# Kernel optimization log

Measured on AMD Instinct MI355X. Metric: run time of the kernel, lower is better.

Reference implementation:

```python
import jax, jax.numpy as jnp
import numpy as np

N = 8192          # total nodes (bipartite: first half left, second half right)
E = 65536         # raw edges
D = 256           # emb_dim
H = 8             # heads
HD = D // H       # head_dim = 32
EAD = 2           # edge_attr_dim


def _init(k, shape, fan_in):
    return (jax.random.normal(k, shape, jnp.float32) / np.sqrt(fan_in)).astype(jnp.float32)


def setup_inputs() -> dict:
    key = jax.random.key(0)
    ks = jax.random.split(key, 16)
    x = jax.random.normal(ks[0], (N, D), jnp.float32)
    src = jax.random.randint(ks[1], (E,), 0, N // 2, jnp.int32)
    dst = jax.random.randint(ks[2], (E,), N // 2, N, jnp.int32)
    edge_index = jnp.stack([src, dst])                       # [2, E]
    edge_attr = jax.random.uniform(ks[3], (E, EAD), jnp.float32)
    query_mask = jax.random.randint(ks[4], (E,), 0, 2, jnp.int32).astype(bool)
    return {
        "x": x,
        "edge_index": edge_index,
        "edge_attr": edge_attr,
        "query_mask": query_mask,
        "start_right": N // 2,
        "W_kqv": _init(ks[5], (D, 3 * D), D), "b_kqv": jnp.zeros((3 * D,), jnp.float32),
        "W_edge": _init(ks[6], (EAD, D), EAD), "b_edge": jnp.zeros((D,), jnp.float32),
        "W_att1": _init(ks[7], (3 * HD, HD), 3 * HD), "b_att1": jnp.zeros((HD,), jnp.float32),
        "W_att2": _init(ks[8], (HD, 1), HD), "b_att2": jnp.zeros((1,), jnp.float32),
        "W_out": _init(ks[9], (D, D), D), "b_out": jnp.zeros((D,), jnp.float32),
        "bn_gamma": jnp.ones((D,), jnp.float32), "bn_beta": jnp.zeros((D,), jnp.float32),
    }


def _build_graph(edge_index, query_mask, n):
    """Replicates MetaGNN.forward edge preprocessing (static, int-only)."""
    ei = np.asarray(edge_index)
    qm = np.asarray(query_mask).astype(bool)
    sup = np.where(~qm)[0]                                   # support edges
    # cat([edge_index[:, support], edge_index.flip(0)], dim=1)
    src = np.concatenate([ei[0, sup], ei[1]])
    dst = np.concatenate([ei[1, sup], ei[0]])
    attr_idx = np.concatenate([sup, np.arange(ei.shape[1])])
    # remove_self_loops
    keep = src != dst
    src, dst, attr_idx = src[keep], dst[keep], attr_idx[keep]
    # add_self_loops with fill_value [0, 0]
    loops = np.arange(n)
    src = np.concatenate([src, loops])
    dst = np.concatenate([dst, loops])
    return jnp.asarray(src), jnp.asarray(dst), jnp.asarray(attr_idx)


def _layer(x, src, dst, ea, W_kqv, b_kqv, W_edge, b_edge, W_att1, b_att1,
           W_att2, b_att2, W_out, b_out, bn_gamma, bn_beta):
    n = x.shape[0]
    kqv = x @ W_kqv + b_kqv                                  # [N, 3D]
    q = kqv[dst, :D].reshape(-1, H, HD)                      # x_i (target)
    k = kqv[src, D:2 * D].reshape(-1, H, HD) / np.sqrt(HD)   # x_j (source)
    v = kqv[src, 2 * D:].reshape(-1, H, HD)
    ef = jax.nn.relu((ea @ W_edge + b_edge).reshape(-1, H, HD))
    feat = jnp.concatenate([k, q, ef], axis=-1)              # [E, H, 3*HD]
    hdn = jax.nn.relu(jnp.einsum('ehf,fd->ehd', feat, W_att1) + b_att1)
    logits = (jnp.einsum('ehd,do->eho', hdn, W_att2) + b_att2)[..., 0]  # [E, H]
    # scatter-softmax over destination node segments
    m = jax.ops.segment_max(logits, dst, num_segments=n)
    a = jnp.exp(logits - m[dst])
    s = jax.ops.segment_sum(a, dst, num_segments=n)
    alpha = a / (s[dst] + 1e-16)                             # [E, H]
    msg = (alpha[..., None] * v).reshape(-1, D) @ W_out + b_out
    out = jax.ops.segment_sum(msg, dst, num_segments=n) + x  # aggr='add' + residual
    # BatchNorm1d (training-mode batch statistics, eps=1e-5)
    mu = out.mean(axis=0)
    var = out.var(axis=0)
    return (out - mu) / jnp.sqrt(var + 1e-5) * bn_gamma + bn_beta


def reference(x, edge_index, edge_attr, query_mask, start_right,
              W_kqv, b_kqv, W_edge, b_edge, W_att1, b_att1, W_att2, b_att2,
              W_out, b_out, bn_gamma, bn_beta):
    n = x.shape[0]
    src, dst, attr_idx = _build_graph(edge_index, query_mask, n)
    ea = jnp.concatenate(
        [edge_attr[attr_idx], jnp.zeros((n, edge_attr.shape[1]), edge_attr.dtype)], axis=0)
    return _layer(x, src, dst, ea, W_kqv, b_kqv, W_edge, b_edge,
                  W_att1, b_att1, W_att2, b_att2, W_out, b_out, bn_gamma, bn_beta)
```

## Files before the change

### kernel.cpp

```cpp
#include <hip/hip_runtime.h>

#define N_NODES 8192
#define E_RAW   65536
#define NSLOT   (2*E_RAW + N_NODES)
#define DEGCAP  48
#define L_ITER  4

typedef __attribute__((ext_vector_type(8)))  short bf16x8;
typedef __attribute__((ext_vector_type(4)))  short bf16x4;
typedef __attribute__((ext_vector_type(4)))  float f32x4;
typedef __attribute__((ext_vector_type(16))) float f32x16;
typedef unsigned short u16;

__device__ __forceinline__ u16 f2b(float f) {
  unsigned u = __float_as_uint(f);
  u = (u + 0x7FFFu + ((u >> 16) & 1u)) >> 16;
  return (u16)u;
}
__device__ __forceinline__ float b2f(u16 b) {
  return __uint_as_float(((unsigned)b) << 16);
}

__global__ __launch_bounds__(256) void setup_k(
    const float* __restrict__ x, u16* __restrict__ xb,
    const float* __restrict__ W_kqv, const float* __restrict__ b_kqv,
    const float* __restrict__ W_att1, const float* __restrict__ b_att1,
    const float* __restrict__ W_edge, const float* __restrict__ b_edge,
    const float* __restrict__ W_out,
    u16* __restrict__ BcatT, float* __restrict__ biascat,
    u16* __restrict__ wa1t, u16* __restrict__ WoutT, float* __restrict__ beW,
    int4* __restrict__ zbase)
{
  __shared__ float tile[64][65];
  const float inv_sqrt_hd = 0.17677669529663687f;
  int bx = blockIdx.x, t = threadIdx.x;

  if (bx < 2048) {
    int i = bx * 256 + t;
    float4 v = ((const float4*)x)[i];
    ushort4 o;
    o.x = f2b(v.x); o.y = f2b(v.y); o.z = f2b(v.z); o.w = f2b(v.w);
    ((ushort4*)xb)[i] = o;
    return;
  }
  if (bx < 2836) {
    int c = bx - 2048;
    int i = t;
    if (c < 768) {
      float v;
      if (c < 256) {
        int h = c >> 5, d2 = c & 31;
        float s = 0.f;
        #pragma unroll
        for (int j = 0; j < 32; ++j)
          s += W_kqv[i*768 + 256 + h*32 + j] * W_att1[j*32 + d2];
        v = s * inv_sqrt_hd;
      } else if (c < 512) {
        int c2 = c - 256; int h = c2 >> 5, d2 = c2 & 31;
        float s = 0.f;
        #pragma unroll
        for (int j = 0; j < 32; ++j)
          s += W_kqv[i*768 + h*32 + j] * W_att1[(32+j)*32 + d2];
        v = s;
      } else {
        v = W_kqv[i*768 + c];
      }
      BcatT[(size_t)c * 256 + i] = f2b(v);
      if (i == 0) {
        float bv;
        if (c < 256) {
          int h = c >> 5, d2 = c & 31;
          float s = 0.f;
          for (int j = 0; j < 32; ++j)
            s += b_kqv[256 + h*32 + j] * W_att1[j*32 + d2];
          bv = s * inv_sqrt_hd;
        } else if (c < 512) {
          int c2 = c - 256; int h = c2 >> 5, d2 = c2 & 31;
          float s = 0.f;
          for (int j = 0; j < 32; ++j)
            s += b_kqv[h*32 + j] * W_att1[(32+j)*32 + d2];
          bv = s + b_att1[c2 & 31];
        } else {
          bv = b_kqv[c];
        }
        biascat[c] = bv;
      }
    } else if (c < 772) {
      int idx = (c - 768) * 256 + i;
      int d2 = idx >> 5, j = idx & 31;
      wa1t[idx] = f2b(W_att1[(64 + j) * 32 + d2]);
    } else {
      int b = c - 772;
      int r0 = (b >> 2) * 64, c0 = (b & 3) * 64;
      for (int idx = i; idx < 4096; idx += 256) {
        int r = idx >> 6, cc = idx & 63;
        tile[r][cc] = W_out[(size_t)(r0 + r) * 256 + c0 + cc];
      }
      __syncthreads();
      for (int idx = i; idx < 4096; idx += 256) {
        int cc = idx >> 6, r = idx & 63;
        WoutT[(size_t)(c0 + cc) * 256 + r0 + r] = f2b(tile[r][cc]);
      }
    }
    return;
  }
  if (bx == 2836) {
    int h = t >> 5, d2 = t & 31;
    float s = 0.f;
    #pragma unroll
    for (int f = 0; f < 32; ++f)
      s += fmaxf(b_edge[h*32 + f], 0.f) * W_att1[(64 + f)*32 + d2];
    beW[h*32 + d2] = s;
    return;
  }
  int i = (bx - 2837) * 256 + t;
  if (i < 2176) zbase[i] = make_int4(0, 0, 0, 0);
}

__global__ __launch_bounds__(256) void gemm_scatter_k(
    const u16* __restrict__ xb, const u16* __restrict__ BcatT,
    const float* __restrict__ biascat, u16* __restrict__ nodeF,
    const int* __restrict__ ei, const int* __restrict__ qm,
    int* __restrict__ cnt, int* __restrict__ csr)
{
  int bx = blockIdx.x, t = threadIdx.x;
  if (bx < 768) {
    int lane = t & 63, wid = t >> 6;
    int cb = bx % 12, rb = bx / 12;
    int r0 = rb * 128 + wid * 32;
    int c0 = cb * 64;
    int lr = lane & 15, lk = (lane >> 4) * 8;
    f32x4 acc0[4] = {}, acc1[4] = {};
    for (int k0 = 0; k0 < 256; k0 += 32) {
      bf16x8 a0 = *(const bf16x8*)&xb[(size_t)(r0 + lr) * 256 + k0 + lk];
      bf16x8 a1 = *(const bf16x8*)&xb[(size_t)(r0 + 16 + lr) * 256 + k0 + lk];
      bf16x8 b0 = *(const bf16x8*)&BcatT[(size_t)(c0 + lr) * 256 + k0 + lk];
      bf16x8 b1 = *(const bf16x8*)&BcatT[(size_t)(c0 + 16 + lr) * 256 + k0 + lk];
      bf16x8 b2 = *(const bf16x8*)&BcatT[(size_t)(c0 + 32 + lr) * 256 + k0 + lk];
      bf16x8 b3 = *(const bf16x8*)&BcatT[(size_t)(c0 + 48 + lr) * 256 + k0 + lk];
      acc0[0] = __builtin_amdgcn_mfma_f32_16x16x32_bf16(a0, b0, acc0[0], 0, 0, 0);
      acc0[1] = __builtin_amdgcn_mfma_f32_16x16x32_bf16(a0, b1, acc0[1], 0, 0, 0);
      acc0[2] = __builtin_amdgcn_mfma_f32_16x16x32_bf16(a0, b2, acc0[2], 0, 0, 0);
      acc0[3] = __builtin_amdgcn_mfma_f32_16x16x32_bf16(a0, b3, acc0[3], 0, 0, 0);
      acc1[0] = __builtin_amdgcn_mfma_f32_16x16x32_bf16(a1, b0, acc1[0], 0, 0, 0);
      acc1[1] = __builtin_amdgcn_mfma_f32_16x16x32_bf16(a1, b1, acc1[1], 0, 0, 0);
      acc1[2] = __builtin_amdgcn_mfma_f32_16x16x32_bf16(a1, b2, acc1[2], 0, 0, 0);
      acc1[3] = __builtin_amdgcn_mfma_f32_16x16x32_bf16(a1, b3, acc1[3], 0, 0, 0);
    }
    int rbase = r0 + (lane >> 4) * 4;
    #pragma unroll
    for (int cc = 0; cc < 4; ++cc) {
      float bias = biascat[c0 + cc*16 + lr];
      #pragma unroll
      for (int r = 0; r < 4; ++r) {
        nodeF[(size_t)(rbase + r) * 768 + c0 + cc*16 + lr]      = f2b(acc0[cc][r] + bias);
        nodeF[(size_t)(rbase + 16 + r) * 768 + c0 + cc*16 + lr] = f2b(acc1[cc][r] + bias);
      }
    }
    return;
  }
  int slot = (bx - 768) * 256 + t;
  if (slot >= NSLOT) return;
  int src, dst;
  if (slot < E_RAW) {
    if (qm[slot] != 0) return;
    src = ei[slot]; dst = ei[E_RAW + slot];
  } else if (slot < 2*E_RAW) {
    int e = slot - E_RAW;
    src = ei[E_RAW + e]; dst = ei[e];
  } else {
    int n = slot - 2*E_RAW;
    src = n; dst = n;
  }
  int pos = atomicAdd(&cnt[dst], 1);
  if (pos < DEGCAP) csr[dst*DEGCAP + pos] = (slot << 13) | src;
}

__global__ __launch_bounds__(256) void logits_k(
    const int* __restrict__ ei, const int* __restrict__ qm,
    const float* __restrict__ eattr, const u16* __restrict__ nf,
    const u16* __restrict__ wa1t,
    const float* __restrict__ W_edge, const float* __restrict__ b_edge,
    const float* __restrict__ W_att2, const float* __restrict__ beW,
    float* __restrict__ lgd)
{
  __shared__ __align__(16) u16 kqls[4][16][8][40];

  int bx = blockIdx.x, t = threadIdx.x, lane = t & 63, wid = t >> 6;
  int col = lane & 31;
  int e = col >> 3, h = col & 7, hi = lane >> 5;

  float w2r[16];
  #pragma unroll
  for (int r = 0; r < 16; ++r)
    w2r[r] = W_att2[(r & 3) + 8*(r >> 2) + 4*hi];

  if (bx < 1024) {
    float ce0[16], ce1[16], cbe[16];
    #pragma unroll
    for (int i = 0; i < 8; ++i) {
      int fA = hi*8 + i, fB = 16 + hi*8 + i;
      ce0[i]   = W_edge[h*32 + fA];       ce0[8+i] = W_edge[h*32 + fB];
      ce1[i]   = W_edge[256 + h*32 + fA]; ce1[8+i] = W_edge[256 + h*32 + fB];
      cbe[i]   = b_edge[h*32 + fA];       cbe[8+i] = b_edge[h*32 + fB];
    }
    bf16x8 af0 = *(const bf16x8*)&wa1t[(lane & 31)*32 + hi*8];
    bf16x8 af1 = *(const bf16x8*)&wa1t[(lane & 31)*32 + 16 + hi*8];

    for (int it = 0; it < L_ITER; ++it) {
      int er0 = ((bx * L_ITER + it) * 4 + wid) * 4;
      int er = er0 + e;
      int eqm = qm[er];
      float2 ea = *(const float2*)&eattr[2*er];

      #pragma unroll
      for (int m = 0; m < 8; ++m) {
        int flat = m*64 + lane;
        int ri = flat >> 5, chunk = flat & 31;
        int ee = ri & 3, ty = ri >> 2;
        int erow = er0 + ee;
        int node = (ty & 1) ? ei[E_RAW + erow] : ei[erow];
        int koff = (ty >> 1) ? 256 : 0;
        bf16x8 v = *(const bf16x8*)&nf[(size_t)node*768 + koff + chunk*8];
        *(bf16x8*)&kqls[wid][ri][chunk >> 2][(chunk & 3)*8] = v;
      }

      bf16x8 bf0, bf1;
      #pragma unroll
      for (int i = 0; i < 8; ++i) {
        float v0 = fmaf(ea.x, ce0[i],   fmaf(ea.y, ce1[i],   cbe[i]));
        float v1 = fmaf(ea.x, ce0[8+i], fmaf(ea.y, ce1[8+i], cbe[8+i]));
        bf0[i] = (short)f2b(fmaxf(v0, 0.f));
        bf1[i] = (short)f2b(fmaxf(v1, 0.f));
      }
      f32x16 acc = {};
      acc = __builtin_amdgcn_mfma_f32_32x32x16_bf16(af0, bf0, acc, 0, 0, 0);
      acc = __builtin_amdgcn_mfma_f32_32x32x16_bf16(af1, bf1, acc, 0, 0, 0);

      __builtin_amdgcn_wave_barrier();

      float lg0 = 0.f, lg1 = 0.f;
      #pragma unroll
      for (int q = 0; q < 4; ++q) {
        int off = q*8 + 4*hi;
        bf16x4 k0 = *(const bf16x4*)&kqls[wid][e][h][off];
        bf16x4 q0 = *(const bf16x4*)&kqls[wid][12 + e][h][off];
        bf16x4 k1 = *(const bf16x4*)&kqls[wid][4 + e][h][off];
        bf16x4 q1 = *(const bf16x4*)&kqls[wid][8 + e][h][off];
        #pragma unroll
        for (int j = 0; j < 4; ++j) {
          int r = q*4 + j;
          float efw = acc[r];
          float p0 = efw + b2f((u16)k0[j]) + b2f((u16)q0[j]);
          float p1 = efw + b2f((u16)k1[j]) + b2f((u16)q1[j]);
          lg0 = fmaf(fmaxf(p0, 0.f), w2r[r], lg0);
          lg1 = fmaf(fmaxf(p1, 0.f), w2r[r], lg1);
        }
      }
      lg0 += __shfl_xor(lg0, 32);
      lg1 += __shfl_xor(lg1, 32);
      if (hi == 0) {
        if (eqm == 0) lgd[(size_t)er*8 + h] = lg0;
        lgd[(size_t)(E_RAW + er)*8 + h] = lg1;
      }
      __builtin_amdgcn_wave_barrier();
    }
  } else {
    float bew[16];
    #pragma unroll
    for (int r = 0; r < 16; ++r)
      bew[r] = beW[h*32 + (r & 3) + 8*(r >> 2) + 4*hi];

    for (int it = 0; it < L_ITER; ++it) {
      int n0 = (((bx - 1024) * L_ITER + it) * 4 + wid) * 4;
      int nn = n0 + e;
      #pragma unroll
      for (int m = 0; m < 4; ++m) {
        int flat = m*64 + lane;
        int ri = flat >> 5, chunk = flat & 31;
        int ee = ri & 3, ty = ri >> 2;
        int node = n0 + ee;
        bf16x8 v = *(const bf16x8*)&nf[(size_t)node*768 + (ty ? 256 : 0) + chunk*8];
        *(bf16x8*)&kqls[wid][ri][chunk >> 2][(chunk & 3)*8] = v;
      }
      __builtin_amdgcn_wave_barrier();
      float lg0 = 0.f;
      #pragma unroll
      for (int q = 0; q < 4; ++q) {
        int off = q*8 + 4*hi;
        bf16x4 k0 = *(const bf16x4*)&kqls[wid][e][h][off];
        bf16x4 q0 = *(const bf16x4*)&kqls[wid][4 + e][h][off];
        #pragma unroll
        for (int j = 0; j < 4; ++j) {
          int r = q*4 + j;
          float p = bew[r] + b2f((u16)k0[j]) + b2f((u16)q0[j]);
          lg0 = fmaf(fmaxf(p, 0.f), w2r[r], lg0);
        }
      }
      lg0 += __shfl_xor(lg0, 32);
      if (hi == 0) lgd[(size_t)(2*E_RAW + nn)*8 + h] = lg0;
      __builtin_amdgcn_wave_barrier();
    }
  }
}

__global__ __launch_bounds__(256) void aggr_k(const int* __restrict__ cnt,
                                              const int* __restrict__ csr,
                                              const float* __restrict__ lgd,
                                              const u16* __restrict__ nf,
                                              u16* __restrict__ aggb) {
  int t = threadIdx.x, lane = t & 63, wid = t >> 6;
  int n = blockIdx.x * 4 + wid;
  int deg = cnt[n]; if (deg > DEGCAP) deg = DEGCAP;

  float m = -3.4e38f, s = 0.f;
  for (int i = lane >> 3; i < deg; i += 8) {
    int pk = csr[n*DEGCAP + i];
    float val = lgd[(size_t)((unsigned)pk >> 13)*8 + (lane & 7)];
    float mn = fmaxf(m, val);
    s = s * __expf(m - mn) + __expf(val - mn);
    m = mn;
  }
  #pragma unroll
  for (int msk = 8; msk <= 32; msk <<= 1) {
    float mo = __shfl_xor(m, msk), so = __shfl_xor(s, msk);
    float mn = fmaxf(m, mo);
    s = s * __expf(m - mn) + so * __expf(mo - mn);
    m = mn;
  }
  float sinv = 1.f / (s + 1e-16f);
  int head = lane >> 3;
  float mh = __shfl(m, head);
  float sh = __shfl(sinv, head);

  float ac0 = 0.f, ac1 = 0.f, ac2 = 0.f, ac3 = 0.f;
  const u16* vb = nf + 512 + lane * 4;
  #pragma unroll 2
  for (int i = 0; i < deg; ++i) {
    int pk = csr[n*DEGCAP + i];
    int slot = (unsigned)pk >> 13, srcv = pk & 8191;
    float a = __expf(lgd[(size_t)slot*8 + head] - mh) * sh;
    bf16x4 v = *(const bf16x4*)&vb[(size_t)srcv * 768];
    ac0 = fmaf(a, b2f((u16)v[0]), ac0);
    ac1 = fmaf(a, b2f((u16)v[1]), ac1);
    ac2 = fmaf(a, b2f((u16)v[2]), ac2);
    ac3 = fmaf(a, b2f((u16)v[3]), ac3);
  }
  ushort4 o; o.x = f2b(ac0); o.y = f2b(ac1); o.z = f2b(ac2); o.w = f2b(ac3);
  *(ushort4*)&aggb[(size_t)n * 256 + lane * 4] = o;
}

__global__ __launch_bounds__(256) void gemmout_k(const u16* __restrict__ aggb,
                                                 const u16* __restrict__ WoutT,
                                                 const float* __restrict__ x,
                                                 const int* __restrict__ cnt,
                                                 const float* __restrict__ b_out,
                                                 float* __restrict__ out,
                                                 float* __restrict__ bnsum,
                                                 float* __restrict__ bnsq) {
  int t = threadIdx.x, lane = t & 63, wid = t >> 6;
  int r0 = (blockIdx.y * 4 + wid) * 32;
  int c0 = blockIdx.x * 32;
  int lr = lane & 15, lk = (lane >> 4) * 8;
  f32x4 acc00 = {0.f,0.f,0.f,0.f}, acc01 = {0.f,0.f,0.f,0.f};
  f32x4 acc10 = {0.f,0.f,0.f,0.f}, acc11 = {0.f,0.f,0.f,0.f};
  for (int k0 = 0; k0 < 256; k0 += 32) {
    bf16x8 a0 = *(const bf16x8*)&aggb[(size_t)(r0 + lr) * 256 + k0 + lk];
    bf16x8 a1 = *(const bf16x8*)&aggb[(size_t)(r0 + 16 + lr) * 256 + k0 + lk];
    bf16x8 b0 = *(const bf16x8*)&WoutT[(size_t)(c0 + lr) * 256 + k0 + lk];
    bf16x8 b1 = *(const bf16x8*)&WoutT[(size_t)(c0 + 16 + lr) * 256 + k0 + lk];
    acc00 = __builtin_amdgcn_mfma_f32_16x16x32_bf16(a0, b0, acc00, 0, 0, 0);
    acc01 = __builtin_amdgcn_mfma_f32_16x16x32_bf16(a0, b1, acc01, 0, 0, 0);
    acc10 = __builtin_amdgcn_mfma_f32_16x16x32_bf16(a1, b0, acc10, 0, 0, 0);
    acc11 = __builtin_amdgcn_mfma_f32_16x16x32_bf16(a1, b1, acc11, 0, 0, 0);
  }
  int colA = c0 + lr, colB = c0 + 16 + lr;
  float bA = b_out[colA], bB = b_out[colB];
  int rbase = r0 + (lane >> 4) * 4;
  float sA = 0.f, qA = 0.f, sB = 0.f, qB = 0.f;
  #pragma unroll
  for (int r = 0; r < 4; ++r) {
    int rowA = rbase + r, rowB = rbase + 16 + r;
    float degA = (float)cnt[rowA], degB = (float)cnt[rowB];
    float v00 = acc00[r] + x[(size_t)rowA * 256 + colA] + degA * bA;
    float v01 = acc01[r] + x[(size_t)rowA * 256 + colB] + degA * bB;
    float v10 = acc10[r] + x[(size_t)rowB * 256 + colA] + degB * bA;
    float v11 = acc11[r] + x[(size_t)rowB * 256 + colB] + degB * bB;
    out[(size_t)rowA * 256 + colA] = v00;
    out[(size_t)rowA * 256 + colB] = v01;
    out[(size_t)rowB * 256 + colA] = v10;
    out[(size_t)rowB * 256 + colB] = v11;
    sA += v00 + v10; qA += v00*v00 + v10*v10;
    sB += v01 + v11; qB += v01*v01 + v11*v11;
  }
  #pragma unroll
  for (int msk = 16; msk <= 32; msk <<= 1) {
    sA += __shfl_xor(sA, msk); qA += __shfl_xor(qA, msk);
    sB += __shfl_xor(sB, msk); qB += __shfl_xor(qB, msk);
  }
  if (lane < 16) {
    atomicAdd(&bnsum[colA], sA); atomicAdd(&bnsq[colA], qA);
    atomicAdd(&bnsum[colB], sB); atomicAdd(&bnsq[colB], qB);
  }
}

__global__ __launch_bounds__(256) void bnapply_k(float* __restrict__ out,
                                                 const float* __restrict__ bnsum,
                                                 const float* __restrict__ bnsq,
                                                 const float* __restrict__ gamma,
                                                 const float* __restrict__ beta) {
  int t = threadIdx.x;
  int c4 = t & 63;
  int r = blockIdx.x * 4 + (t >> 6);
  float4 s4 = ((const float4*)bnsum)[c4];
  float4 q4 = ((const float4*)bnsq)[c4];
  float4 g4 = ((const float4*)gamma)[c4];
  float4 b4 = ((const float4*)beta)[c4];
  float4 v = ((const float4*)out)[(size_t)r * 64 + c4];
  #pragma unroll
  for (int j = 0; j < 4; ++j) {
    float mu = (&s4.x)[j] * (1.f / 8192.f);
    float var = (&q4.x)[j] * (1.f / 8192.f) - mu*mu;
    float inv = rsqrtf(var + 1e-5f);
    (&v.x)[j] = ((&v.x)[j] - mu) * inv * (&g4.x)[j] + (&b4.x)[j];
  }
  ((float4*)out)[(size_t)r * 64 + c4] = v;
}

extern "C" void kernel_launch(void* const* d_in, const int* in_sizes, int n_in,
                              void* d_out, int out_size, void* d_ws, size_t ws_size,
                              hipStream_t stream) {
  (void)in_sizes; (void)n_in; (void)out_size; (void)ws_size;
  const float* x      = (const float*)d_in[0];
  const int*   ei     = (const int*)d_in[1];
  const float* eattr  = (const float*)d_in[2];
  const int*   qm     = (const int*)d_in[3];
  const float* W_kqv  = (const float*)d_in[5];
  const float* b_kqv  = (const float*)d_in[6];
  const float* W_edge = (const float*)d_in[7];
  const float* b_edge = (const float*)d_in[8];
  const float* W_att1 = (const float*)d_in[9];
  const float* b_att1 = (const float*)d_in[10];
  const float* W_att2 = (const float*)d_in[11];
  const float* W_out  = (const float*)d_in[13];
  const float* b_out  = (const float*)d_in[14];
  const float* gamma  = (const float*)d_in[15];
  const float* beta   = (const float*)d_in[16];
  float* out = (float*)d_out;

  char* w = (char*)d_ws;
  u16*    xb      = (u16*)w;     w += (size_t)N_NODES*256*2;
  u16*    BcatT   = (u16*)w;     w += (size_t)768*256*2;
  u16*    wa1t    = (u16*)w;     w += 1024*2;
  u16*    WoutT   = (u16*)w;     w += (size_t)256*256*2;
  u16*    nodeFb  = (u16*)w;     w += (size_t)N_NODES*768*2;
  float*  biascat = (float*)w;   w += 768*4;
  float*  beW     = (float*)w;   w += 256*4;
  u16*    aggb    = (u16*)w;     w += (size_t)N_NODES*256*2;
  int*    cnt     = (int*)w;     w += N_NODES*4;
  float*  bnsum   = (float*)w;   w += 256*4;
  float*  bnsq    = (float*)w;   w += 256*4;
  int*    csr     = (int*)w;     w += (size_t)N_NODES*DEGCAP*4;
  float*  lgd     = (float*)w;   w += (size_t)NSLOT*8*4;

  setup_k<<<2846, 256, 0, stream>>>(
      x, xb, W_kqv, b_kqv, W_att1, b_att1, W_edge, b_edge, W_out,
      BcatT, biascat, wa1t, WoutT, beW, (int4*)cnt);

  gemm_scatter_k<<<768 + (NSLOT + 255)/256, 256, 0, stream>>>(
      xb, BcatT, biascat, nodeFb, ei, qm, cnt, csr);

  logits_k<<<1024 + 128, 256, 0, stream>>>(ei, qm, eattr, nodeFb, wa1t,
                                           W_edge, b_edge, W_att2, beW, lgd);

  aggr_k<<<N_NODES/4, 256, 0, stream>>>(cnt, csr, lgd, nodeFb, aggb);

  gemmout_k<<<dim3(256/32, N_NODES/128), 256, 0, stream>>>(
      aggb, WoutT, x, cnt, b_out, out, bnsum, bnsq);

  bnapply_k<<<N_NODES/4, 256, 0, stream>>>(out, bnsum, bnsq, gamma, beta);
}
```

Measured before the change: 102.0 us.

## Prefetch gathers in logits and aggregation kernels, widen output GEMM tile

The logits kernel loads edge attributes and query flags up front and fetches the next iteration's node indices early, so gather latency overlaps compute. The aggregation kernel reads each node's CSR list once into registers, broadcasts entries by shuffle, and software-pipelines the next logit/value load. The output GEMM now computes 64 columns per wave, reusing A fragments across four B tiles and halving the grid. This costs more registers, which may reduce occupancy, and leaves fewer blocks for the GEMM.

```diff
diff --git a/kernel.cpp b/kernel.cpp
--- a/kernel.cpp
+++ b/kernel.cpp
@@ -207,24 +207,44 @@
     bf16x8 af0 = *(const bf16x8*)&wa1t[(lane & 31)*32 + hi*8];
     bf16x8 af1 = *(const bf16x8*)&wa1t[(lane & 31)*32 + 16 + hi*8];
 
+    int eqm_r[L_ITER]; float2 ea_r[L_ITER];
+    #pragma unroll
     for (int it = 0; it < L_ITER; ++it) {
-      int er0 = ((bx * L_ITER + it) * 4 + wid) * 4;
-      int er = er0 + e;
-      int eqm = qm[er];
-      float2 ea = *(const float2*)&eattr[2*er];
-
+      int er = ((bx * L_ITER + it) * 4 + wid) * 4 + e;
+      eqm_r[it] = qm[er];
+      ea_r[it] = *(const float2*)&eattr[2*er];
+    }
+
+    int nidx[2][8];
+    #pragma unroll
+    for (int m = 0; m < 8; ++m) {
+      int flat = m*64 + lane, ri = flat >> 5;
+      int ee = ri & 3, ty = ri >> 2;
+      int erow = ((bx * L_ITER + 0) * 4 + wid) * 4 + ee;
+      nidx[0][m] = (ty & 1) ? ei[E_RAW + erow] : ei[erow];
+    }
+
+    #pragma unroll
+    for (int it = 0; it < L_ITER; ++it) {
+      if (it + 1 < L_ITER) {
+        #pragma unroll
+        for (int m = 0; m < 8; ++m) {
+          int flat = m*64 + lane, ri = flat >> 5;
+          int ee = ri & 3, ty = ri >> 2;
+          int erow = ((bx * L_ITER + it + 1) * 4 + wid) * 4 + ee;
+          nidx[(it+1) & 1][m] = (ty & 1) ? ei[E_RAW + erow] : ei[erow];
+        }
+      }
       #pragma unroll
       for (int m = 0; m < 8; ++m) {
-        int flat = m*64 + lane;
-        int ri = flat >> 5, chunk = flat & 31;
-        int ee = ri & 3, ty = ri >> 2;
-        int erow = er0 + ee;
-        int node = (ty & 1) ? ei[E_RAW + erow] : ei[erow];
+        int flat = m*64 + lane, ri = flat >> 5, chunk = flat & 31;
+        int ty = ri >> 2;
         int koff = (ty >> 1) ? 256 : 0;
-        bf16x8 v = *(const bf16x8*)&nf[(size_t)node*768 + koff + chunk*8];
+        bf16x8 v = *(const bf16x8*)&nf[(size_t)nidx[it & 1][m]*768 + koff + chunk*8];
         *(bf16x8*)&kqls[wid][ri][chunk >> 2][(chunk & 3)*8] = v;
       }
 
+      float2 ea = ea_r[it];
       bf16x8 bf0, bf1;
       #pragma unroll
       for (int i = 0; i < 8; ++i) {
@@ -260,7 +280,8 @@
       lg0 += __shfl_xor(lg0, 32);
       lg1 += __shfl_xor(lg1, 32);
       if (hi == 0) {
-        if (eqm == 0) lgd[(size_t)er*8 + h] = lg0;
+        int er = ((bx * L_ITER + it) * 4 + wid) * 4 + e;
+        if (eqm_r[it] == 0) lgd[(size_t)er*8 + h] = lg0;
         lgd[(size_t)(E_RAW + er)*8 + h] = lg1;
       }
       __builtin_amdgcn_wave_barrier();
@@ -312,13 +333,22 @@
   int t = threadIdx.x, lane = t & 63, wid = t >> 6;
   int n = blockIdx.x * 4 + wid;
   int deg = cnt[n]; if (deg > DEGCAP) deg = DEGCAP;
-
+  int head = lane >> 3;
+
+  int pk = (lane < deg) ? csr[n*DEGCAP + lane] : 0;
+
+  int i0 = lane >> 3, hh = lane & 7;
+  int nit = (deg + 7) >> 3;
   float m = -3.4e38f, s = 0.f;
-  for (int i = lane >> 3; i < deg; i += 8) {
-    int pk = csr[n*DEGCAP + i];
-    float val = lgd[(size_t)((unsigned)pk >> 13)*8 + (lane & 7)];
+  for (int ii = 0; ii < nit; ++ii) {
+    int i = ii * 8 + i0;
+    int ic = (i < deg) ? i : 0;
+    int pki = __shfl(pk, ic);
+    float val = (i < deg)
+        ? lgd[(size_t)((unsigned)pki >> 13)*8 + hh] : -3.4e38f;
     float mn = fmaxf(m, val);
-    s = s * __expf(m - mn) + __expf(val - mn);
+    float addv = (i < deg) ? __expf(val - mn) : 0.f;
+    s = s * __expf(m - mn) + addv;
     m = mn;
   }
   #pragma unroll
@@ -329,18 +359,23 @@
     m = mn;
   }
   float sinv = 1.f / (s + 1e-16f);
-  int head = lane >> 3;
   float mh = __shfl(m, head);
   float sh = __shfl(sinv, head);
 
   float ac0 = 0.f, ac1 = 0.f, ac2 = 0.f, ac3 = 0.f;
   const u16* vb = nf + 512 + lane * 4;
-  #pragma unroll 2
+  int pk0 = __shfl(pk, 0);
+  float lg_pf = lgd[(size_t)((unsigned)pk0 >> 13)*8 + head];
+  bf16x4 v_pf = *(const bf16x4*)&vb[(size_t)(pk0 & 8191) * 768];
   for (int i = 0; i < deg; ++i) {
-    int pk = csr[n*DEGCAP + i];
-    int slot = (unsigned)pk >> 13, srcv = pk & 8191;
-    float a = __expf(lgd[(size_t)slot*8 + head] - mh) * sh;
-    bf16x4 v = *(const bf16x4*)&vb[(size_t)srcv * 768];
+    float lgv = lg_pf;
+    bf16x4 v = v_pf;
+    if (i + 1 < deg) {
+      int pkn = __shfl(pk, i + 1);
+      lg_pf = lgd[(size_t)((unsigned)pkn >> 13)*8 + head];
+      v_pf = *(const bf16x4*)&vb[(size_t)(pkn & 8191) * 768];
+    }
+    float a = __expf(lgv - mh) * sh;
     ac0 = fmaf(a, b2f((u16)v[0]), ac0);
     ac1 = fmaf(a, b2f((u16)v[1]), ac1);
     ac2 = fmaf(a, b2f((u16)v[2]), ac2);
@@ -359,48 +394,56 @@
                                                  float* __restrict__ bnsum,
                                                  float* __restrict__ bnsq) {
   int t = threadIdx.x, lane = t & 63, wid = t >> 6;
-  int r0 = (blockIdx.y * 4 + wid) * 32;
-  int c0 = blockIdx.x * 32;
+  int bx = blockIdx.x;
+  int cb = bx & 3, rb = bx >> 2;
+  int r0 = rb * 128 + wid * 32;
+  int c0 = cb * 64;
   int lr = lane & 15, lk = (lane >> 4) * 8;
-  f32x4 acc00 = {0.f,0.f,0.f,0.f}, acc01 = {0.f,0.f,0.f,0.f};
-  f32x4 acc10 = {0.f,0.f,0.f,0.f}, acc11 = {0.f,0.f,0.f,0.f};
+  f32x4 acc0[4] = {}, acc1[4] = {};
   for (int k0 = 0; k0 < 256; k0 += 32) {
     bf16x8 a0 = *(const bf16x8*)&aggb[(size_t)(r0 + lr) * 256 + k0 + lk];
     bf16x8 a1 = *(const bf16x8*)&aggb[(size_t)(r0 + 16 + lr) * 256 + k0 + lk];
     bf16x8 b0 = *(const bf16x8*)&WoutT[(size_t)(c0 + lr) * 256 + k0 + lk];
     bf16x8 b1 = *(const bf16x8*)&WoutT[(size_t)(c0 + 16 + lr) * 256 + k0 + lk];
-    acc00 = __builtin_amdgcn_mfma_f32_16x16x32_bf16(a0, b0, acc00, 0, 0, 0);
-    acc01 = __builtin_amdgcn_mfma_f32_16x16x32_bf16(a0, b1, acc01, 0, 0, 0);
-    acc10 = __builtin_amdgcn_mfma_f32_16x16x32_bf16(a1, b0, acc10, 0, 0, 0);
-    acc11 = __builtin_amdgcn_mfma_f32_16x16x32_bf16(a1, b1, acc11, 0, 0, 0);
-  }
-  int colA = c0 + lr, colB = c0 + 16 + lr;
-  float bA = b_out[colA], bB = b_out[colB];
+    bf16x8 b2 = *(const bf16x8*)&WoutT[(size_t)(c0 + 32 + lr) * 256 + k0 + lk];
+    bf16x8 b3 = *(const bf16x8*)&WoutT[(size_t)(c0 + 48 + lr) * 256 + k0 + lk];
+    acc0[0] = __builtin_amdgcn_mfma_f32_16x16x32_bf16(a0, b0, acc0[0], 0, 0, 0);
+    acc0[1] = __builtin_amdgcn_mfma_f32_16x16x32_bf16(a0, b1, acc0[1], 0, 0, 0);
+    acc0[2] = __builtin_amdgcn_mfma_f32_16x16x32_bf16(a0, b2, acc0[2], 0, 0, 0);
+    acc0[3] = __builtin_amdgcn_mfma_f32_16x16x32_bf16(a0, b3, acc0[3], 0, 0, 0);
+    acc1[0] = __builtin_amdgcn_mfma_f32_16x16x32_bf16(a1, b0, acc1[0], 0, 0, 0);
+    acc1[1] = __builtin_amdgcn_mfma_f32_16x16x32_bf16(a1, b1, acc1[1], 0, 0, 0);
+    acc1[2] = __builtin_amdgcn_mfma_f32_16x16x32_bf16(a1, b2, acc1[2], 0, 0, 0);
+    acc1[3] = __builtin_amdgcn_mfma_f32_16x16x32_bf16(a1, b3, acc1[3], 0, 0, 0);
+  }
   int rbase = r0 + (lane >> 4) * 4;
-  float sA = 0.f, qA = 0.f, sB = 0.f, qB = 0.f;
+  float degA[4], degB[4];
   #pragma unroll
   for (int r = 0; r < 4; ++r) {
-    int rowA = rbase + r, rowB = rbase + 16 + r;
-    float degA = (float)cnt[rowA], degB = (float)cnt[rowB];
-    float v00 = acc00[r] + x[(size_t)rowA * 256 + colA] + degA * bA;
-    float v01 = acc01[r] + x[(size_t)rowA * 256 + colB] + degA * bB;
-    float v10 = acc10[r] + x[(size_t)rowB * 256 + colA] + degB * bA;
-    float v11 = acc11[r] + x[(size_t)rowB * 256 + colB] + degB * bB;
-    out[(size_t)rowA * 256 + colA] = v00;
-    out[(size_t)rowA * 256 + colB] = v01;
-    out[(size_t)rowB * 256 + colA] = v10;
-    out[(size_t)rowB * 256 + colB] = v11;
-    sA += v00 + v10; qA += v00*v00 + v10*v10;
-    sB += v01 + v11; qB += v01*v01 + v11*v11;
+    degA[r] = (float)cnt[rbase + r];
+    degB[r] = (float)cnt[rbase + 16 + r];
   }
   #pragma unroll
-  for (int msk = 16; msk <= 32; msk <<= 1) {
-    sA += __shfl_xor(sA, msk); qA += __shfl_xor(qA, msk);
-    sB += __shfl_xor(sB, msk); qB += __shfl_xor(qB, msk);
-  }
-  if (lane < 16) {
-    atomicAdd(&bnsum[colA], sA); atomicAdd(&bnsq[colA], qA);
-    atomicAdd(&bnsum[colB], sB); atomicAdd(&bnsq[colB], qB);
+  for (int cc = 0; cc < 4; ++cc) {
+    int colC = c0 + cc*16 + lr;
+    float bC = b_out[colC];
+    float sC = 0.f, qC = 0.f;
+    #pragma unroll
+    for (int r = 0; r < 4; ++r) {
+      int rowA = rbase + r, rowB = rbase + 16 + r;
+      float v0 = acc0[cc][r] + x[(size_t)rowA * 256 + colC] + degA[r] * bC;
+      float v1 = acc1[cc][r] + x[(size_t)rowB * 256 + colC] + degB[r] * bC;
+      out[(size_t)rowA * 256 + colC] = v0;
+      out[(size_t)rowB * 256 + colC] = v1;
+      sC += v0 + v1; qC += v0*v0 + v1*v1;
+    }
+    #pragma unroll
+    for (int msk = 16; msk <= 32; msk <<= 1) {
+      sC += __shfl_xor(sC, msk); qC += __shfl_xor(qC, msk);
+    }
+    if (lane < 16) {
+      atomicAdd(&bnsum[colC], sC); atomicAdd(&bnsq[colC], qC);
+    }
   }
 }
 
@@ -475,7 +518,7 @@
 
   aggr_k<<<N_NODES/4, 256, 0, stream>>>(cnt, csr, lgd, nodeFb, aggb);
 
-  gemmout_k<<<dim3(256/32, N_NODES/128), 256, 0, stream>>>(
+  gemmout_k<<<256, 256, 0, stream>>>(
       aggb, WoutT, x, cnt, b_out, out, bnsum, bnsq);
 
   bnapply_k<<<N_NODES/4, 256, 0, stream>>>(out, bnsum, bnsq, gamma, beta);
```

Result: faster. 94.99 us (-6.9%).
